# Kernel tuning notes

Hardware: AMD Instinct MI355X
Metric: run time of the kernel (lower is better)

## Reference

```python
import jax, jax.numpy as jnp
import numpy as np

N_LABELS = 48
L = N_LABELS + 2            # labels + stop + start
START = N_LABELS + 1
STOP = N_LABELS
NEG = -10000.0
B, T = 512, 1024


def setup_inputs() -> dict:
    key = jax.random.key(0)
    k1, k2, k3 = jax.random.split(key, 3)
    feats = jax.random.normal(k1, (B, T, L), dtype=jnp.float32)
    lens = jax.random.randint(k2, (B,), 1, T + 1, dtype=jnp.int32)
    transitions = jax.random.normal(k3, (L, L), dtype=jnp.float32)
    return {"feats": feats, "lens": lens, "transitions": transitions}


def reference(feats, lens, transitions):
    # Viterbi decode (module's forward). feats: [B, T, L]
    b, t, l = feats.shape
    vit0 = jnp.full((b, l), NEG, feats.dtype).at[:, START].set(0.0)

    def step(carry, logit):
        vit, c = carry                                   # vit [B,L], c [B]
        scores = vit[:, None, :] + transitions[None, :, :]   # [B, to, from]
        vt_max = scores.max(2)                           # [B, L]
        ptr = scores.argmax(2)                           # [B, L] backpointers
        vit_nxt = vt_max + logit
        vit_new = jnp.where((c > 0)[:, None], vit_nxt, vit)
        # add stop transition exactly when this is the last real timestep
        vit_new = vit_new + jnp.where((c == 1)[:, None], transitions[STOP][None, :], 0.0)
        return (vit_new, c - 1), ptr

    (vit, _), pointers = jax.lax.scan(step, (vit0, lens), jnp.swapaxes(feats, 0, 1))
    scores = vit.max(1)                                  # [B]
    idx = vit.argmax(1)                                  # [B]

    barange = jnp.arange(b)

    def back(i, ptr):
        ni = ptr[barange, i]
        return ni, ni

    _, back_seq = jax.lax.scan(back, idx, pointers, reverse=True)  # back_seq[t] = idx after ptr_t
    # original drops the earliest backtracked index (belongs to the virtual start step)
    paths = jnp.concatenate([back_seq[1:], idx[None]], axis=0).T   # [B, T]
    return scores, paths
```

## Files before the change

kernel.cpp:

```cpp
#include <hip/hip_runtime.h>

typedef unsigned char u8;

#define TT 1024
#define BB 512
#define LL 50
#define STOPI 48
#define STARTI 49
#define NEGV -10000.0f

#define PTR_OFF 4096

#define ROW_ADDS(ROWP, S, TRR)                                                 \
    {                                                                          \
        _Pragma("unroll")                                                      \
        for (int k_ = 0; k_ < 13; ++k_) {                                      \
            const float4 q_ = *(const float4*)((ROWP) + 4 * k_);               \
            const int j_ = 4 * k_;                                             \
            (S)[j_ + 0] = q_.x + (TRR)[j_ + 0];                                \
            (S)[j_ + 1] = q_.y + (TRR)[j_ + 1];                                \
            if (j_ + 2 < LL) (S)[j_ + 2] = q_.z + (TRR)[j_ + 2];               \
            if (j_ + 3 < LL) (S)[j_ + 3] = q_.w + (TRR)[j_ + 3];               \
        }                                                                      \
    }

#define MAX50(S, M)                                                            \
    {                                                                          \
        float r0_[17];                                                         \
        _Pragma("unroll")                                                      \
        for (int k_ = 0; k_ < 16; ++k_)                                        \
            r0_[k_] = fmaxf(fmaxf((S)[3*k_], (S)[3*k_+1]), (S)[3*k_+2]);       \
        r0_[16] = fmaxf((S)[48], (S)[49]);                                     \
        float r1_[6];                                                          \
        _Pragma("unroll")                                                      \
        for (int k_ = 0; k_ < 5; ++k_)                                         \
            r1_[k_] = fmaxf(fmaxf(r0_[3*k_], r0_[3*k_+1]), r0_[3*k_+2]);       \
        r1_[5] = fmaxf(r0_[15], r0_[16]);                                      \
        (M) = fmaxf(fmaxf(fmaxf(r1_[0], r1_[1]), r1_[2]),                      \
                    fmaxf(fmaxf(r1_[3], r1_[4]), r1_[5]));                     \
    }

#define ARGMAX50(S, BI)                                                        \
    {                                                                          \
        float b0_=-3.4e38f, b1_=-3.4e38f, b2_=-3.4e38f, b3_=-3.4e38f;          \
        int   i0_=0, i1_=13, i2_=26, i3_=39;                                   \
        _Pragma("unroll")                                                      \
        for (int j_=0;  j_<13; ++j_){ const float v_=(S)[j_]; if (v_>b0_){b0_=v_;i0_=j_;} } \
        _Pragma("unroll")                                                      \
        for (int j_=13; j_<26; ++j_){ const float v_=(S)[j_]; if (v_>b1_){b1_=v_;i1_=j_;} } \
        _Pragma("unroll")                                                      \
        for (int j_=26; j_<39; ++j_){ const float v_=(S)[j_]; if (v_>b2_){b2_=v_;i2_=j_;} } \
        _Pragma("unroll")                                                      \
        for (int j_=39; j_<50; ++j_){ const float v_=(S)[j_]; if (v_>b3_){b3_=v_;i3_=j_;} } \
        if (b1_>b0_){b0_=b1_;i0_=i1_;}                                         \
        if (b2_>b0_){b0_=b2_;i0_=i2_;}                                         \
        if (b3_>b0_){b0_=b3_;i0_=i3_;}                                         \
        (BI) = i0_;                                                            \
    }

#define PROCESS_GROUP(BASE)                                                    \
    {                                                                          \
        if (!have && (BASE) + 3 > len) {                                       \
            const float* rowp_ = &ring[len & 15][0];                           \
            float s_[LL];                                                      \
            ROW_ADDS(rowp_, s_, trr)                                           \
            ARGMAX50(s_, cidx)                                                 \
            have = true;                                                       \
        }                                                                      \
        unsigned pk_ = 0;                                                      \
        _Pragma("unroll 1")                                                    \
        for (int r_ = 0; r_ < 4; ++r_) {                                       \
            const int t_ = (BASE) + r_;                                        \
            int idx_;                                                          \
            if (t_ <= len) {                                                   \
                const float* rowp_ = &ring[t_ & 15][0];                        \
                float s_[LL];                                                  \
                ROW_ADDS(rowp_, s_, trr)                                       \
                ARGMAX50(s_, idx_)                                             \
            } else {                                                           \
                idx_ = cidx;                                                   \
            }                                                                  \
            pk_ |= (unsigned)idx_ << (8 * r_);                                 \
        }                                                                      \
        if (lane < LL) *(unsigned*)(pt + (BASE)) = pk_;                        \
    }

__global__ __launch_bounds__(192, 2) void viterbi_fused(
    const float* __restrict__ feats, const int* __restrict__ lens,
    const float* __restrict__ trans, float* __restrict__ out_scores,
    int* __restrict__ idx_ws, u8* __restrict__ ptr_ws)
{
    const int b    = blockIdx.x;
    const int tid  = threadIdx.x;
    const int lane = tid & 63;
    const int w    = __builtin_amdgcn_readfirstlane(tid >> 6);
    const int row  = (lane < LL) ? lane : (LL - 1);

    __shared__ float ring[16][64];

    float trr[LL];
#pragma unroll
    for (int j = 0; j < LL; ++j) trr[j] = trans[row * LL + j];
    const int len = lens[b];

    if (w == 0) {
        const float tr_stop = trans[STOPI * LL + row];
        float vit = (lane == STARTI) ? 0.0f : NEGV;
        const float* fb = feats + (size_t)b * (TT * LL);

        float f[8];
#pragma unroll
        for (int i = 0; i < 8; ++i) f[i] = fb[i * LL + row];

        for (int it = 0; it < 128; ++it) {
#pragma unroll
            for (int i = 0; i < 8; ++i) {
                const int t = (it << 3) + i;
                float* rowp = &ring[t & 15][0];
                if (t <= len) {
                    if (lane < LL) rowp[lane] = vit;
                }
                if (t < len) {
                    float s[LL];
                    ROW_ADDS(rowp, s, trr)
                    float m; MAX50(s, m)
                    float nv = m + f[i];
                    if (t == len - 1) nv += tr_stop;
                    vit = nv;
                    int tp = t + 8; if (tp > TT - 1) tp = TT - 1;
                    f[i] = fb[(size_t)tp * LL + row];
                }
            }
            asm volatile("s_waitcnt lgkmcnt(0)" ::: "memory");
            __builtin_amdgcn_s_barrier();
            asm volatile("" ::: "memory");
        }

        float m = -3.4e38f; int mi = 0;
#pragma unroll
        for (int j = 0; j < LL; ++j) {
            float sv = __int_as_float(__builtin_amdgcn_readlane(__float_as_int(vit), j));
            if (sv > m) { m = sv; mi = j; }
        }
        if (lane == 0) { out_scores[b] = m; idx_ws[b] = mi; }
    } else {
        u8* pt = ptr_ws + (size_t)b * (TT * LL) + (size_t)row * TT;
        int  cidx = 0;
        bool have = false;

        for (int it = 0; it < 128; ++it) {
            if (it > 0) {
                const int base = ((it - 1) << 3) + ((w - 1) << 2);
                PROCESS_GROUP(base)
            }
            asm volatile("s_waitcnt lgkmcnt(0)" ::: "memory");
            __builtin_amdgcn_s_barrier();
            asm volatile("" ::: "memory");
        }
        {
            const int base = (127 << 3) + ((w - 1) << 2);
            PROCESS_GROUP(base)
        }
    }
}

#define LSW(S, T) (((S) << 10) + ((T) ^ (((S) & 31) << 2)))

__global__ __launch_bounds__(64) void viterbi_bwd(
    const int* __restrict__ idx_ws, const u8* __restrict__ ptr_ws,
    float* __restrict__ out_paths)
{
    const int b = blockIdx.x;
    const int lane = threadIdx.x;

    __shared__ u8 lptr[TT * LL];
    __shared__ u8 maps[32 * LL];
    __shared__ int entries[33];

    {
        const unsigned* src = (const unsigned*)(ptr_ws + (size_t)b * TT * LL);
        unsigned* dst = (unsigned*)lptr;
        for (int i = lane; i < (TT * LL) / 4; i += 64) {
            const int to = i >> 8;
            const int t4 = i & 255;
            dst[(to << 8) + (t4 ^ (to & 31))] = src[i];
        }
    }
    __syncthreads();

    {
        int st[25], tt[25], cidx[25];
#pragma unroll
        for (int k = 0; k < 25; ++k) {
            int ww = k * 64 + lane;
            int c = ww / 50;
            int l = ww - c * 50;
            st[k] = l;
            tt[k] = c * 32 + 31;
            cidx[k] = c * 50 + l;
        }
        for (int j = 0; j < 32; ++j) {
#pragma unroll
            for (int k = 0; k < 25; ++k) {
                st[k] = lptr[LSW(st[k], tt[k])];
                tt[k] -= 1;
            }
        }
#pragma unroll
        for (int k = 0; k < 25; ++k) maps[cidx[k]] = (u8)st[k];
    }
    __syncthreads();

    const int idx = idx_ws[b];

    if (lane == 0) {
        int i = idx;
        for (int c = 31; c >= 0; --c) {
            entries[c + 1] = i;
            i = maps[c * 50 + i];
        }
        entries[0] = i;
    }
    __syncthreads();

    float* po = out_paths + (size_t)b * TT;
    if (lane < 32) {
        const int c = lane;
        int s = entries[c + 1];
        for (int j = 0; j < 32; ++j) {
            int t = c * 32 + 31 - j;
            int ni = lptr[LSW(s, t)];
            if (t > 0) po[t - 1] = (float)ni;
            s = ni;
        }
    }
    if (lane == 0) po[TT - 1] = (float)idx;
}

extern "C" void kernel_launch(void* const* d_in, const int* in_sizes, int n_in,
                              void* d_out, int out_size, void* d_ws, size_t ws_size,
                              hipStream_t stream) {
    const float* feats = (const float*)d_in[0];
    const int*   lens  = (const int*)d_in[1];
    const float* trans = (const float*)d_in[2];

    float* scores = (float*)d_out;
    float* paths  = scores + BB;

    int* idx_ws = (int*)d_ws;
    u8*  ptr_ws = (u8*)d_ws + PTR_OFF;

    viterbi_fused<<<BB, 192, 0, stream>>>(feats, lens, trans, scores, idx_ws, ptr_ws);
    viterbi_bwd<<<BB, 64, 0, stream>>>(idx_ws, ptr_ws, paths);
}
```

Measured before the change: 570.2 us.

## Fuse forward and backtrace into one kernel with LDS-resident backpointers

Merges the forward Viterbi kernel and the backtrace kernel into a single kernel that keeps the byte backpointer table in shared memory, so the global workspace write and read-back are removed. The forward loop now stops after the sequence's actual length instead of running all 1024 steps, and the tail of the pointer table is filled with the constant final-argmax pattern. The forward wave broadcasts vit with readlane instead of reading the ring from LDS, and it raises its scheduling priority. Argmax is rewritten as a max followed by an equality scan. The trade-off is about 52KB of LDS per block, which may lower occupancy below the two-block launch bound.

```diff
diff --git a/kernel.cpp b/kernel.cpp
--- a/kernel.cpp
+++ b/kernel.cpp
@@ -9,20 +9,8 @@
 #define STARTI 49
 #define NEGV -10000.0f
 
-#define PTR_OFF 4096
-
-#define ROW_ADDS(ROWP, S, TRR)                                                 \
-    {                                                                          \
-        _Pragma("unroll")                                                      \
-        for (int k_ = 0; k_ < 13; ++k_) {                                      \
-            const float4 q_ = *(const float4*)((ROWP) + 4 * k_);               \
-            const int j_ = 4 * k_;                                             \
-            (S)[j_ + 0] = q_.x + (TRR)[j_ + 0];                                \
-            (S)[j_ + 1] = q_.y + (TRR)[j_ + 1];                                \
-            if (j_ + 2 < LL) (S)[j_ + 2] = q_.z + (TRR)[j_ + 2];               \
-            if (j_ + 3 < LL) (S)[j_ + 3] = q_.w + (TRR)[j_ + 3];               \
-        }                                                                      \
-    }
+#define PDW(TO, T4) (((TO) << 8) + ((T4) ^ ((TO) & 31)))
+#define PBYTE(S, T) ((((S) << 10) + (((((T) >> 2) ^ ((S) & 31))) << 2)) + ((T) & 3))
 
 #define MAX50(S, M)                                                            \
     {                                                                          \
@@ -40,55 +28,54 @@
                     fmaxf(fmaxf(r1_[3], r1_[4]), r1_[5]));                     \
     }
 
-#define ARGMAX50(S, BI)                                                        \
-    {                                                                          \
-        float b0_=-3.4e38f, b1_=-3.4e38f, b2_=-3.4e38f, b3_=-3.4e38f;          \
-        int   i0_=0, i1_=13, i2_=26, i3_=39;                                   \
-        _Pragma("unroll")                                                      \
-        for (int j_=0;  j_<13; ++j_){ const float v_=(S)[j_]; if (v_>b0_){b0_=v_;i0_=j_;} } \
-        _Pragma("unroll")                                                      \
-        for (int j_=13; j_<26; ++j_){ const float v_=(S)[j_]; if (v_>b1_){b1_=v_;i1_=j_;} } \
-        _Pragma("unroll")                                                      \
-        for (int j_=26; j_<39; ++j_){ const float v_=(S)[j_]; if (v_>b2_){b2_=v_;i2_=j_;} } \
-        _Pragma("unroll")                                                      \
-        for (int j_=39; j_<50; ++j_){ const float v_=(S)[j_]; if (v_>b3_){b3_=v_;i3_=j_;} } \
-        if (b1_>b0_){b0_=b1_;i0_=i1_;}                                         \
-        if (b2_>b0_){b0_=b2_;i0_=i2_;}                                         \
-        if (b3_>b0_){b0_=b3_;i0_=i3_;}                                         \
-        (BI) = i0_;                                                            \
+#define ROW_ADDS(ROWP, S)                                                      \
+    {                                                                          \
+        _Pragma("unroll")                                                      \
+        for (int k_ = 0; k_ < 13; ++k_) {                                      \
+            const float4 q_ = *(const float4*)((ROWP) + 4 * k_);               \
+            const int j_ = 4 * k_;                                             \
+            (S)[j_ + 0] = q_.x + trr[j_ + 0];                                  \
+            (S)[j_ + 1] = q_.y + trr[j_ + 1];                                  \
+            if (j_ + 2 < LL) (S)[j_ + 2] = q_.z + trr[j_ + 2];                 \
+            if (j_ + 3 < LL) (S)[j_ + 3] = q_.w + trr[j_ + 3];                 \
+        }                                                                      \
+    }
+
+#define ROWIDX(T, IOUT)                                                        \
+    {                                                                          \
+        const float* rowp_ = &ring[(T) & 15][0];                               \
+        float a_[LL];                                                          \
+        ROW_ADDS(rowp_, a_)                                                    \
+        float m_; MAX50(a_, m_)                                                \
+        int ii_ = 0;                                                           \
+        _Pragma("unroll")                                                      \
+        for (int j_ = LL - 1; j_ >= 0; --j_)                                   \
+            if (a_[j_] == m_) ii_ = j_;                                        \
+        (IOUT) = ii_;                                                          \
     }
 
 #define PROCESS_GROUP(BASE)                                                    \
     {                                                                          \
-        if (!have && (BASE) + 3 > len) {                                       \
-            const float* rowp_ = &ring[len & 15][0];                           \
-            float s_[LL];                                                      \
-            ROW_ADDS(rowp_, s_, trr)                                           \
-            ARGMAX50(s_, cidx)                                                 \
-            have = true;                                                       \
-        }                                                                      \
         unsigned pk_ = 0;                                                      \
         _Pragma("unroll 1")                                                    \
         for (int r_ = 0; r_ < 4; ++r_) {                                       \
             const int t_ = (BASE) + r_;                                        \
             int idx_;                                                          \
             if (t_ <= len) {                                                   \
-                const float* rowp_ = &ring[t_ & 15][0];                        \
-                float s_[LL];                                                  \
-                ROW_ADDS(rowp_, s_, trr)                                       \
-                ARGMAX50(s_, idx_)                                             \
+                ROWIDX(t_, idx_)                                               \
             } else {                                                           \
+                if (!have) { ROWIDX(len, cidx) have = true; }                  \
                 idx_ = cidx;                                                   \
             }                                                                  \
             pk_ |= (unsigned)idx_ << (8 * r_);                                 \
         }                                                                      \
-        if (lane < LL) *(unsigned*)(pt + (BASE)) = pk_;                        \
-    }
-
-__global__ __launch_bounds__(192, 2) void viterbi_fused(
+        if (lane < LL)                                                         \
+            ((unsigned*)lptr)[PDW(row, (BASE) >> 2)] = pk_;                    \
+    }
+
+__global__ __launch_bounds__(192, 2) void viterbi_all(
     const float* __restrict__ feats, const int* __restrict__ lens,
-    const float* __restrict__ trans, float* __restrict__ out_scores,
-    int* __restrict__ idx_ws, u8* __restrict__ ptr_ws)
+    const float* __restrict__ trans, float* __restrict__ out)
 {
     const int b    = blockIdx.x;
     const int tid  = threadIdx.x;
@@ -97,13 +84,23 @@
     const int row  = (lane < LL) ? lane : (LL - 1);
 
     __shared__ float ring[16][64];
+    __shared__ u8    lptr[TT * LL];
+    __shared__ u8    maps[32 * LL];
+    __shared__ int   entries[33];
+    __shared__ int   fidx;
 
     float trr[LL];
 #pragma unroll
     for (int j = 0; j < LL; ++j) trr[j] = trans[row * LL + j];
-    const int len = lens[b];
+#pragma unroll
+    for (int j = 0; j < LL; ++j) asm("" : "+v"(trr[j]));
+
+    const int len  = lens[b];
+    const int nit0 = (len >> 3) + 1;
+    const int nit  = nit0 > 128 ? 128 : nit0;
 
     if (w == 0) {
+        __builtin_amdgcn_s_setprio(1);
         const float tr_stop = trans[STOPI * LL + row];
         float vit = (lane == STARTI) ? 0.0f : NEGV;
         const float* fb = feats + (size_t)b * (TT * LL);
@@ -112,18 +109,20 @@
 #pragma unroll
         for (int i = 0; i < 8; ++i) f[i] = fb[i * LL + row];
 
-        for (int it = 0; it < 128; ++it) {
+        for (int it = 0; it < nit; ++it) {
 #pragma unroll
             for (int i = 0; i < 8; ++i) {
                 const int t = (it << 3) + i;
-                float* rowp = &ring[t & 15][0];
                 if (t <= len) {
-                    if (lane < LL) rowp[lane] = vit;
+                    if (lane < LL) ring[t & 15][lane] = vit;
                 }
                 if (t < len) {
-                    float s[LL];
-                    ROW_ADDS(rowp, s, trr)
-                    float m; MAX50(s, m)
+                    float a[LL];
+#pragma unroll
+                    for (int j = 0; j < LL; ++j)
+                        a[j] = __int_as_float(__builtin_amdgcn_readlane(
+                                   __float_as_int(vit), j)) + trr[j];
+                    float m; MAX50(a, m)
                     float nv = m + f[i];
                     if (t == len - 1) nv += tr_stop;
                     vit = nv;
@@ -135,6 +134,7 @@
             __builtin_amdgcn_s_barrier();
             asm volatile("" ::: "memory");
         }
+        __builtin_amdgcn_s_setprio(0);
 
         float m = -3.4e38f; int mi = 0;
 #pragma unroll
@@ -142,13 +142,12 @@
             float sv = __int_as_float(__builtin_amdgcn_readlane(__float_as_int(vit), j));
             if (sv > m) { m = sv; mi = j; }
         }
-        if (lane == 0) { out_scores[b] = m; idx_ws[b] = mi; }
+        if (lane == 0) { out[b] = m; fidx = mi; }
     } else {
-        u8* pt = ptr_ws + (size_t)b * (TT * LL) + (size_t)row * TT;
         int  cidx = 0;
         bool have = false;
 
-        for (int it = 0; it < 128; ++it) {
+        for (int it = 0; it < nit; ++it) {
             if (it > 0) {
                 const int base = ((it - 1) << 3) + ((w - 1) << 2);
                 PROCESS_GROUP(base)
@@ -157,63 +156,62 @@
             __builtin_amdgcn_s_barrier();
             asm volatile("" ::: "memory");
         }
-        {
-            const int base = (127 << 3) + ((w - 1) << 2);
-            PROCESS_GROUP(base)
-        }
-    }
-}
-
-#define LSW(S, T) (((S) << 10) + ((T) ^ (((S) & 31) << 2)))
-
-__global__ __launch_bounds__(64) void viterbi_bwd(
-    const int* __restrict__ idx_ws, const u8* __restrict__ ptr_ws,
-    float* __restrict__ out_paths)
-{
-    const int b = blockIdx.x;
-    const int lane = threadIdx.x;
-
-    __shared__ u8 lptr[TT * LL];
-    __shared__ u8 maps[32 * LL];
-    __shared__ int entries[33];
+
+        const int base0 = (nit - 1) << 3;
+        PROCESS_GROUP(base0 + ((w - 1) << 2))
+
+        const int t0f = base0 + 8;
+        if (t0f < TT) {
+            if (!have) { ROWIDX(len, cidx) have = true; }
+            if (lane < LL) {
+                const unsigned pat = (unsigned)cidx * 0x01010101u;
+                int tq = t0f;
+                if (tq & 8) {
+                    if (w == 1) {
+                        ((unsigned*)lptr)[PDW(row, tq >> 2)]     = pat;
+                        ((unsigned*)lptr)[PDW(row, (tq >> 2)+1)] = pat;
+                    }
+                    tq += 8;
+                }
+                for (int t4 = (tq >> 2) + (w - 1) * 4; t4 < 256; t4 += 8) {
+                    ((unsigned*)lptr)[PDW(row, t4 + 0)] = pat;
+                    ((unsigned*)lptr)[PDW(row, t4 + 1)] = pat;
+                    ((unsigned*)lptr)[PDW(row, t4 + 2)] = pat;
+                    ((unsigned*)lptr)[PDW(row, t4 + 3)] = pat;
+                }
+            }
+        }
+    }
+
+    __syncthreads();
 
     {
-        const unsigned* src = (const unsigned*)(ptr_ws + (size_t)b * TT * LL);
-        unsigned* dst = (unsigned*)lptr;
-        for (int i = lane; i < (TT * LL) / 4; i += 64) {
-            const int to = i >> 8;
-            const int t4 = i & 255;
-            dst[(to << 8) + (t4 ^ (to & 31))] = src[i];
-        }
+        int st[9], ttt[9], ci[9];
+#pragma unroll
+        for (int k = 0; k < 9; ++k) {
+            int id = tid + 192 * k;
+            int valid = id < 1600;
+            int idc = valid ? id : 1599;
+            int c = idc / 50;
+            int l = idc - c * 50;
+            st[k] = l; ttt[k] = c * 32 + 31; ci[k] = valid ? idc : -1;
+        }
+        for (int j = 0; j < 32; ++j) {
+#pragma unroll
+            for (int k = 0; k < 9; ++k) {
+                st[k] = lptr[PBYTE(st[k], ttt[k])];
+                ttt[k] -= 1;
+            }
+        }
+#pragma unroll
+        for (int k = 0; k < 9; ++k)
+            if (ci[k] >= 0) maps[ci[k]] = (u8)st[k];
     }
     __syncthreads();
 
-    {
-        int st[25], tt[25], cidx[25];
-#pragma unroll
-        for (int k = 0; k < 25; ++k) {
-            int ww = k * 64 + lane;
-            int c = ww / 50;
-            int l = ww - c * 50;
-            st[k] = l;
-            tt[k] = c * 32 + 31;
-            cidx[k] = c * 50 + l;
-        }
-        for (int j = 0; j < 32; ++j) {
-#pragma unroll
-            for (int k = 0; k < 25; ++k) {
-                st[k] = lptr[LSW(st[k], tt[k])];
-                tt[k] -= 1;
-            }
-        }
-#pragma unroll
-        for (int k = 0; k < 25; ++k) maps[cidx[k]] = (u8)st[k];
-    }
-    __syncthreads();
-
-    const int idx = idx_ws[b];
-
-    if (lane == 0) {
+    const int idx = fidx;
+
+    if (tid == 0) {
         int i = idx;
         for (int c = 31; c >= 0; --c) {
             entries[c + 1] = i;
@@ -223,18 +221,18 @@
     }
     __syncthreads();
 
-    float* po = out_paths + (size_t)b * TT;
-    if (lane < 32) {
-        const int c = lane;
+    float* po = out + BB + (size_t)b * TT;
+    if (tid < 32) {
+        const int c = tid;
         int s = entries[c + 1];
         for (int j = 0; j < 32; ++j) {
             int t = c * 32 + 31 - j;
-            int ni = lptr[LSW(s, t)];
+            int ni = lptr[PBYTE(s, t)];
             if (t > 0) po[t - 1] = (float)ni;
             s = ni;
         }
     }
-    if (lane == 0) po[TT - 1] = (float)idx;
+    if (tid == 0) po[TT - 1] = (float)idx;
 }
 
 extern "C" void kernel_launch(void* const* d_in, const int* in_sizes, int n_in,
@@ -244,12 +242,5 @@
     const int*   lens  = (const int*)d_in[1];
     const float* trans = (const float*)d_in[2];
 
-    float* scores = (float*)d_out;
-    float* paths  = scores + BB;
-
-    int* idx_ws = (int*)d_ws;
-    u8*  ptr_ws = (u8*)d_ws + PTR_OFF;
-
-    viterbi_fused<<<BB, 192, 0, stream>>>(feats, lens, trans, scores, idx_ws, ptr_ws);
-    viterbi_bwd<<<BB, 64, 0, stream>>>(idx_ws, ptr_ws, paths);
+    viterbi_all<<<BB, 192, 0, stream>>>(feats, lens, trans, (float*)d_out);
 }
```

Result: no change. 562.5 us (-1.4%).
